# Performance work log

Hardware: AMD Instinct MI355X
Metric: run time of the kernel (lower is better)

Reference implementation:

```python
import jax, jax.numpy as jnp
import numpy as np

B, T, C, H = 2, 2048, 1024, 16
DK = DV = C // H  # 64
CONV_K = 4
EPS = 1e-5


def _causal_depthwise_conv(x, w):
    # x: [B, T, D], w: [D, K]; causal depthwise short convolution
    K = w.shape[1]
    xp = jnp.pad(x, ((0, 0), (K - 1, 0), (0, 0)))
    y = jax.lax.conv_general_dilated(
        xp.transpose(0, 2, 1), w[:, None, :], window_strides=(1,),
        padding='VALID', feature_group_count=w.shape[0])
    return y.transpose(0, 2, 1)


def _l2norm(x):
    return x * jax.lax.rsqrt(jnp.sum(x * x, axis=-1, keepdims=True) + 1e-6)


def _rope(x, rot_dim, base=10000.0):
    # x: [B, H, T, D]; rotate first rot_dim dims (partial_rotary_factor=0.5)
    t = x.shape[2]
    half = rot_dim // 2
    inv_freq = base ** (-jnp.arange(half, dtype=jnp.float32) / half)
    ang = jnp.arange(t, dtype=jnp.float32)[:, None] * inv_freq[None, :]
    cos, sin = jnp.cos(ang), jnp.sin(ang)
    x1 = x[..., :half]; x2 = x[..., half:rot_dim]; xpass = x[..., rot_dim:]
    return jnp.concatenate([x1 * cos - x2 * sin, x2 * cos + x1 * sin, xpass], axis=-1)


def setup_inputs() -> dict:
    key = jax.random.key(0)
    ks = jax.random.split(key, 16)
    s = 0.02
    inp = {
        'x': jax.random.normal(ks[0], (B, T, C), jnp.float32),
        'Wq': jax.random.normal(ks[1], (C, H * DK), jnp.float32) * s,
        'Wk': jax.random.normal(ks[2], (C, H * DK), jnp.float32) * s,
        'Wv': jax.random.normal(ks[3], (C, H * DV), jnp.float32) * s,
        'Wo': jax.random.normal(ks[4], (H * DV, C), jnp.float32) * s,
        'Wg': jax.random.normal(ks[5], (C, H * DV), jnp.float32) * s,
        'Wgk': jax.random.normal(ks[6], (C, H), jnp.float32) * s,
        'Wb': jax.random.normal(ks[7], (C, H), jnp.float32) * s,
        'bb': jnp.zeros((H,), jnp.float32),
        'A_log': jnp.log(jax.random.uniform(ks[8], (H,), jnp.float32, 0.5, 8.0)),
        'conv_q_w': jax.random.normal(ks[10], (H * DK, CONV_K), jnp.float32) * 0.2,
        'conv_k_w': jax.random.normal(ks[11], (H * DK, CONV_K), jnp.float32) * 0.2,
        'conv_v_w': jax.random.normal(ks[12], (H * DV, CONV_K), jnp.float32) * 0.2,
        'gnorm_w': jnp.ones((DV,), jnp.float32),
    }
    dt = jnp.exp(jax.random.uniform(ks[9], (H,), jnp.float32) * (np.log(0.1) - np.log(0.001)) + np.log(0.001))
    dt = jnp.clip(dt, 1e-4, None)
    inp['dt_bias'] = dt + jnp.log(-jnp.expm1(-dt))
    return inp


def reference(x, Wq, Wk, Wv, Wo, Wg, Wgk, Wb, bb, A_log, conv_q_w, conv_k_w, conv_v_w, gnorm_w, dt_bias):
    b, t, c = x.shape
    # projections + causal short conv + silu
    q = jax.nn.silu(_causal_depthwise_conv(x @ Wq, conv_q_w))
    k = jax.nn.silu(_causal_depthwise_conv(x @ Wk, conv_k_w))
    v = jax.nn.silu(_causal_depthwise_conv(x @ Wv, conv_v_w))
    # mamba-style per-head log forget gate and delta-rule learning rate beta
    gk = -jnp.exp(A_log) * jax.nn.softplus(x @ Wgk + dt_bias)   # [B, T, H]
    beta = jax.nn.sigmoid(x @ Wb + bb)                          # [B, T, H]
    q = q.reshape(b, t, H, DK).transpose(0, 2, 1, 3)
    k = k.reshape(b, t, H, DK).transpose(0, 2, 1, 3)
    v = v.reshape(b, t, H, DV).transpose(0, 2, 1, 3)
    q = _rope(_l2norm(q), DK // 2)
    k = _rope(_l2norm(k), DK // 2)
    # gated delta-rule recurrence: S_t = exp(g_t) S_{t-1} + k_t (beta_t (v_t - S^T k_t))^T
    def step(S, ins):
        q_t, k_t, v_t, g_t, b_t = ins
        S = S * jnp.exp(g_t)[..., None, None]
        pred = jnp.einsum('bhk,bhkv->bhv', k_t, S)
        delta = b_t[..., None] * (v_t - pred)
        S = S + k_t[..., None] * delta[..., None, :]
        o_t = jnp.einsum('bhk,bhkv->bhv', q_t, S)
        return S, o_t
    S0 = jnp.zeros((b, H, DK, DV), jnp.float32)
    ins = (q.transpose(2, 0, 1, 3), k.transpose(2, 0, 1, 3), v.transpose(2, 0, 1, 3),
           gk.transpose(1, 0, 2), beta.transpose(1, 0, 2))
    _, o = jax.lax.scan(step, S0, ins)          # o: [T, B, H, DV]
    o = o.transpose(1, 0, 2, 3)                 # [B, T, H, DV]
    # fused RMSNorm + swish gate, then output projection
    g = (x @ Wg).reshape(b, t, H, DV)
    o = o * jax.lax.rsqrt(jnp.mean(o * o, axis=-1, keepdims=True) + EPS)
    o = o * gnorm_w * jax.nn.silu(g)
    return o.reshape(b, t, H * DV) @ Wo
```

## Files before the change

kernel.cpp:

```cpp
#include <hip/hip_runtime.h>
#include <math.h>

typedef float f32x4 __attribute__((ext_vector_type(4)));
typedef __bf16 bf16x8 __attribute__((ext_vector_type(8)));
typedef __bf16 bf16x4 __attribute__((ext_vector_type(4)));

static constexpr int NB = 2, NT = 2048, NC = 1024, NH = 16, ND = 64;
static constexpr int NM = NB * NT;

__device__ inline float rdlane(float v, int l) {
  return __builtin_bit_cast(float, __builtin_amdgcn_readlane(__builtin_bit_cast(int, v), l));
}

__global__ __launch_bounds__(256) void k_convert(const float* __restrict__ src,
                                                 __bf16* __restrict__ dst, int n4) {
  int i = blockIdx.x * 256 + threadIdx.x;
  if (i >= n4) return;
  float4 v = ((const float4*)src)[i];
  bf16x4 o;
  o.x = (__bf16)v.x; o.y = (__bf16)v.y; o.z = (__bf16)v.z; o.w = (__bf16)v.w;
  ((bf16x4*)dst)[i] = o;
}

__global__ __launch_bounds__(256) void k_transpose(const float* __restrict__ src,
                                                   __bf16* __restrict__ dst) {
  __shared__ float t[64][65];
  int r0 = blockIdx.y * 64, c0 = blockIdx.x * 64;
  int lr = threadIdx.x >> 6;
  int lc = threadIdx.x & 63;
#pragma unroll
  for (int j = 0; j < 16; j++) {
    int r = j * 4 + lr;
    t[r][lc] = src[(size_t)(r0 + r) * 1024 + c0 + lc];
  }
  __syncthreads();
#pragma unroll
  for (int j = 0; j < 16; j++) {
    int r = j * 4 + lr;
    dst[(size_t)(c0 + r) * 1024 + r0 + lc] = (__bf16)t[lc][r];
  }
}

__global__ __launch_bounds__(256) void k_buildwgb(const float* __restrict__ Wgk,
    const float* __restrict__ Wb, __bf16* __restrict__ wgb_t) {
  int k0 = blockIdx.x * 64;
  int tid = threadIdx.x;
  int n = tid >> 3;
  int kk = (tid & 7) * 8;
  const float* src = n < 16 ? &Wgk[n] : &Wb[n - 16];
#pragma unroll
  for (int i = 0; i < 8; i++) {
    int k = k0 + kk + i;
    wgb_t[(size_t)n * 1024 + k] = (__bf16)src[(size_t)k * 16];
  }
  for (int i = tid; i < 6144; i += 256)
    wgb_t[32 * 1024 + (size_t)blockIdx.x * 6144 + i] = (__bf16)0.f;
}

__global__ __launch_bounds__(256) void k_gemm(const __bf16* __restrict__ A,
    const __bf16* B0, const __bf16* B1, const __bf16* B2, const __bf16* B3,
    const __bf16* B4, float* C0, float* C1, float* C2, float* C3, float* C4,
    int nblkPer) {
  constexpr int Kd = 1024;
  int mblk = blockIdx.x;
  int yb = blockIdx.y;
  int sel = yb / nblkPer;
  int nb = yb % nblkPer;
  const __bf16* Bt = sel == 0 ? B0 : sel == 1 ? B1 : sel == 2 ? B2 : sel == 3 ? B3 : B4;
  float* Cp = sel == 0 ? C0 : sel == 1 ? C1 : sel == 2 ? C2 : sel == 3 ? C3 : C4;
  int ldc = sel == 4 ? 128 : 1024;

  __shared__ __bf16 As[128 * 32];
  __shared__ __bf16 Bs[128 * 32];
  int tid = threadIdx.x;
  int lane = tid & 63;
  int w = tid >> 6;
  int wr = w >> 1, wc = w & 1;

  f32x4 acc[4][4];
#pragma unroll
  for (int r = 0; r < 4; r++)
#pragma unroll
    for (int c = 0; c < 4; c++) acc[r][c] = (f32x4){0.f, 0.f, 0.f, 0.f};

  int rowh = tid >> 2;
  int kcol = (tid & 3) * 8;
  const __bf16* aS = A + (size_t)(mblk * 128 + rowh) * Kd + kcol;
  const __bf16* bS = Bt + (size_t)(nb * 128 + rowh) * Kd + kcol;
  int rbase = (wr * 64 + (lane & 15)) * 32 + ((lane >> 4) * 8);
  int cbase = (wc * 64 + (lane & 15)) * 32 + ((lane >> 4) * 8);

  for (int kt = 0; kt < Kd; kt += 32) {
    uint4 a0 = *(const uint4*)(aS + kt);
    uint4 a1 = *(const uint4*)(aS + (size_t)64 * Kd + kt);
    uint4 b0 = *(const uint4*)(bS + kt);
    uint4 b1 = *(const uint4*)(bS + (size_t)64 * Kd + kt);
    __syncthreads();
    *(uint4*)&As[rowh * 32 + kcol] = a0;
    *(uint4*)&As[(rowh + 64) * 32 + kcol] = a1;
    *(uint4*)&Bs[rowh * 32 + kcol] = b0;
    *(uint4*)&Bs[(rowh + 64) * 32 + kcol] = b1;
    __syncthreads();
    bf16x8 af[4], bfr[4];
#pragma unroll
    for (int r = 0; r < 4; r++) af[r] = *(const bf16x8*)&As[rbase + r * 16 * 32];
#pragma unroll
    for (int c = 0; c < 4; c++) bfr[c] = *(const bf16x8*)&Bs[cbase + c * 16 * 32];
#pragma unroll
    for (int r = 0; r < 4; r++)
#pragma unroll
      for (int c = 0; c < 4; c++)
        acc[r][c] = __builtin_amdgcn_mfma_f32_16x16x32_bf16(af[r], bfr[c], acc[r][c], 0, 0, 0);
  }
  int orow = mblk * 128 + wr * 64 + ((lane >> 4) << 2);
  int ocol = nb * 128 + wc * 64 + (lane & 15);
#pragma unroll
  for (int r = 0; r < 4; r++)
#pragma unroll
    for (int c = 0; c < 4; c++)
#pragma unroll
      for (int j = 0; j < 4; j++)
        Cp[(size_t)(orow + r * 16 + j) * ldc + ocol + c * 16] = acc[r][c][j];
}

__global__ __launch_bounds__(256) void k_projpost(const float* __restrict__ pbuf,
    const float* __restrict__ bb, const float* __restrict__ A_log,
    const float* __restrict__ dtb, float* __restrict__ gk_arr,
    float* __restrict__ beta_arr) {
  int idx = blockIdx.x * 256 + threadIdx.x;
  int m = idx >> 5, j = idx & 31;
  int b = m >> 11, t = m & 2047;
  float v = pbuf[(size_t)m * 128 + j];
  if (j < 16) {
    float z = v + dtb[j];
    float sp = z > 20.f ? z : log1pf(__expf(z));
    gk_arr[((size_t)(b * 16 + j)) * 2048 + t] = -__expf(A_log[j]) * sp;
  } else {
    int jj = j - 16;
    float z = v + bb[jj];
    beta_arr[((size_t)(b * 16 + jj)) * 2048 + t] = 1.f / (1.f + __expf(-z));
  }
}

__global__ __launch_bounds__(256) void k_conv(
    const float* __restrict__ qpre, const float* __restrict__ kpre,
    const float* __restrict__ vpre, const float* __restrict__ cqw,
    const float* __restrict__ ckw, const float* __restrict__ cvw,
    float* __restrict__ qhat, float* __restrict__ khat, float* __restrict__ vhat) {
  int z = blockIdx.z;
  const float* src = z == 0 ? qpre : z == 1 ? kpre : vpre;
  const float* cw = z == 0 ? cqw : z == 1 ? ckw : cvw;
  float* dst = z == 0 ? qhat : z == 1 ? khat : vhat;
  int t0 = blockIdx.x * 64;
  int bh = blockIdx.y;
  int b = bh >> 4, h = bh & 15;
  int tid = threadIdx.x;
  __shared__ float tile[67 * 64];
  __shared__ float outb[64 * 64];
  for (int i = tid; i < 67 * 64; i += 256) {
    int r = i >> 6, c = i & 63;
    int t = t0 - 3 + r;
    tile[i] = (t >= 0) ? src[((size_t)(b * 2048 + t)) * 1024 + h * 64 + c] : 0.f;
  }
  __syncthreads();
  int c = tid & 63;
  int rb = (tid >> 6) * 16;
  float4 w4 = *(const float4*)&cw[(h * 64 + c) * 4];
  size_t obase = ((size_t)bh) * 2048 * 64;
#pragma unroll
  for (int rr = 0; rr < 16; rr++) {
    int r = rb + rr;
    float y = tile[r * 64 + c] * w4.x + tile[(r + 1) * 64 + c] * w4.y +
              tile[(r + 2) * 64 + c] * w4.z + tile[(r + 3) * 64 + c] * w4.w;
    float sv = y * (1.f / (1.f + __expf(-y)));
    if (z == 2) dst[obase + (size_t)(t0 + r) * 64 + c] = sv;
    else outb[r * 64 + c] = sv;
  }
  if (z == 2) return;
  __syncthreads();
  int r = tid >> 2;
  int p = tid & 3;
  float ss = 0.f;
#pragma unroll
  for (int i2 = 0; i2 < 16; i2++) { float vv = outb[r * 64 + p * 16 + i2]; ss += vv * vv; }
  ss += __shfl_xor(ss, 1);
  ss += __shfl_xor(ss, 2);
  float inv = rsqrtf(ss + 1e-6f);
  int tg = t0 + r;
#pragma unroll
  for (int i2 = 0; i2 < 16; i2++) {
    int cc = p * 16 + i2;
    float val = outb[r * 64 + cc] * inv;
    float res;
    if (cc < 16) {
      float x2 = outb[r * 64 + cc + 16] * inv;
      float ang = tg * __expf(-0.5756462732485114f * cc);
      float sn, cn; sincosf(ang, &sn, &cn);
      res = val * cn - x2 * sn;
    } else if (cc < 32) {
      float x1 = outb[r * 64 + cc - 16] * inv;
      float ang = tg * __expf(-0.5756462732485114f * (cc - 16));
      float sn, cn; sincosf(ang, &sn, &cn);
      res = val * cn + x1 * sn;
    } else res = val;
    dst[obase + (size_t)tg * 64 + cc] = res;
  }
}

__global__ __launch_bounds__(256) void k_chunkA(
    const float* __restrict__ khat, const float* __restrict__ vhat,
    const float* __restrict__ gk_arr, const float* __restrict__ beta_arr,
    float* __restrict__ cumbuf, float* __restrict__ Ubuf, float* __restrict__ Wbuf) {
  int bid = blockIdx.x;
  int bh = bid >> 5, ch = bid & 31;
  int tid = threadIdx.x;
  int lane = tid & 63, w = tid >> 6;
  __shared__ __bf16 Kbf[64 * 64];
  __shared__ __attribute__((aligned(16))) float Msh[64 * 68];
  __shared__ float cumsh[64], bsh[64];
  size_t kbase = (size_t)bh * (2048 * 64) + (size_t)ch * 4096;
  size_t gb = (size_t)bh * 2048 + ch * 64;
  size_t cb4096 = (size_t)(bh * 32 + ch) * 4096;

  {
    int row = tid >> 2, c16 = (tid & 3) * 16;
    const float* src = &khat[kbase + row * 64 + c16];
    float4 f0 = *(const float4*)(src + 0);
    float4 f1 = *(const float4*)(src + 4);
    float4 f2 = *(const float4*)(src + 8);
    float4 f3 = *(const float4*)(src + 12);
    bf16x8 h0, h1;
    h0[0] = (__bf16)f0.x; h0[1] = (__bf16)f0.y; h0[2] = (__bf16)f0.z; h0[3] = (__bf16)f0.w;
    h0[4] = (__bf16)f1.x; h0[5] = (__bf16)f1.y; h0[6] = (__bf16)f1.z; h0[7] = (__bf16)f1.w;
    h1[0] = (__bf16)f2.x; h1[1] = (__bf16)f2.y; h1[2] = (__bf16)f2.z; h1[3] = (__bf16)f2.w;
    h1[4] = (__bf16)f3.x; h1[5] = (__bf16)f3.y; h1[6] = (__bf16)f3.z; h1[7] = (__bf16)f3.w;
    int ch0 = ((c16 >> 3) + 0) ^ (row & 7);
    int ch1 = ((c16 >> 3) + 1) ^ (row & 7);
    *(bf16x8*)&Kbf[row * 64 + ch0 * 8] = h0;
    *(bf16x8*)&Kbf[row * 64 + ch1 * 8] = h1;
  }
  for (int i = tid; i < 64 * 68; i += 256) Msh[i] = 0.f;
  if (tid < 64) {
    float g = gk_arr[gb + tid];
    float bv = beta_arr[gb + tid];
#pragma unroll
    for (int d = 1; d < 64; d <<= 1) {
      float n = __shfl_up(g, d, 64);
      if (tid >= d) g += n;
    }
    cumsh[tid] = g;
    bsh[tid] = bv;
    cumbuf[(size_t)(bh * 32 + ch) * 64 + tid] = g;
  }
  __syncthreads();

  {
    f32x4 macc[4];
#pragma unroll
    for (int c = 0; c < 4; c++) macc[c] = (f32x4){0.f, 0.f, 0.f, 0.f};
    int arow = w * 16 + (lane & 15);
    int kb = lane >> 4;
    bf16x8 af0 = *(const bf16x8*)&Kbf[arow * 64 + ((0 + kb) ^ (arow & 7)) * 8];
    bf16x8 af1 = *(const bf16x8*)&Kbf[arow * 64 + ((4 + kb) ^ (arow & 7)) * 8];
#pragma unroll
    for (int c = 0; c < 4; c++) {
      if (c <= w) {
        int brow = c * 16 + (lane & 15);
        bf16x8 bf0 = *(const bf16x8*)&Kbf[brow * 64 + ((0 + kb) ^ (brow & 7)) * 8];
        bf16x8 bf1 = *(const bf16x8*)&Kbf[brow * 64 + ((4 + kb) ^ (brow & 7)) * 8];
        macc[c] = __builtin_amdgcn_mfma_f32_16x16x32_bf16(af0, bf0, macc[c], 0, 0, 0);
        macc[c] = __builtin_amdgcn_mfma_f32_16x16x32_bf16(af1, bf1, macc[c], 0, 0, 0);
      }
    }
    float bt[4], ct[4];
#pragma unroll
    for (int j = 0; j < 4; j++) {
      int trow = w * 16 + (lane >> 4) * 4 + j;
      bt[j] = bsh[trow];
      ct[j] = cumsh[trow];
    }
#pragma unroll
    for (int c = 0; c < 4; c++) {
      if (c <= w) {
        int scol = c * 16 + (lane & 15);
        float cums = cumsh[scol];
#pragma unroll
        for (int j = 0; j < 4; j++) {
          int trow = w * 16 + (lane >> 4) * 4 + j;
          float val = macc[c][j] * bt[j] * __expf(ct[j] - cums);
          Msh[trow * 68 + scol] = (scol < trow) ? val : 0.f;
        }
      }
    }
  }

  float uw[64];
  int c = tid;
  if (tid < 128) {
    bool isU = c < 64;
    int cc = c & 63;
    const float* src = isU ? &vhat[kbase + cc] : &khat[kbase + cc];
#pragma unroll
    for (int t = 0; t < 64; t++) {
      float r = src[t * 64] * bsh[t];
      if (!isU) r *= __expf(cumsh[t]);
      uw[t] = r;
    }
  }
  __syncthreads();

  if (tid < 128) {
#pragma unroll
    for (int t = 1; t < 64; t++) {
      float acc = 0.f;
#pragma unroll
      for (int q = 0; q <= (t - 1) >> 2; q++) {
        float4 m4 = *(const float4*)&Msh[t * 68 + q * 4];
        acc += m4.x * uw[q * 4 + 0] + m4.y * uw[q * 4 + 1] +
               m4.z * uw[q * 4 + 2] + m4.w * uw[q * 4 + 3];
      }
      uw[t] -= acc;
    }
    bool isU = c < 64;
    int cc = c & 63;
    float* dst = isU ? &Ubuf[cb4096 + cc] : &Wbuf[cb4096 + cc];
#pragma unroll
    for (int t = 0; t < 64; t++) dst[t * 64] = uw[t];
  }
}

__global__ __launch_bounds__(256) void k_chunkB(
    const float* __restrict__ khat, const float* __restrict__ cumbuf,
    const float* __restrict__ Ubuf, const float* __restrict__ Wbuf,
    float* __restrict__ Sch) {
  int bid = blockIdx.x;
  int bh = bid >> 3, vb = bid & 7;
  int tid = threadIdx.x;
  int lane = tid & 63, q_ = tid >> 6;
  int c0 = vb * 8 + q_ * 2;
  __shared__ float Ksh[64 * 68];
  float S0 = 0.f, S1 = 0.f;
  for (int ch = 0; ch < 32; ch++) {
    size_t cb = (size_t)(bh * 32 + ch);
    size_t kbase = (size_t)bh * (2048 * 64) + (size_t)ch * 4096;
    __syncthreads();
#pragma unroll
    for (int n4 = 0; n4 < 4; n4++) {
      int n = tid + n4 * 256;
      float4 kv = *(const float4*)&khat[kbase + (size_t)n * 4];
      int row = n >> 4, col = (n & 15) * 4;
      *(float4*)&Ksh[row * 68 + col] = kv;
    }
    float cumv = cumbuf[cb * 64 + lane];
    float cum63 = rdlane(cumv, 63);
    float sc = __expf(cum63 - cumv);
    float Gend = __expf(cum63);
    float2 uv = *(const float2*)&Ubuf[cb * 4096 + (size_t)lane * 64 + c0];
    float Wrow[64];
#pragma unroll
    for (int i4 = 0; i4 < 16; i4++) {
      float4 wv = *(const float4*)&Wbuf[cb * 4096 + (size_t)lane * 64 + i4 * 4];
      Wrow[i4 * 4 + 0] = wv.x; Wrow[i4 * 4 + 1] = wv.y;
      Wrow[i4 * 4 + 2] = wv.z; Wrow[i4 * 4 + 3] = wv.w;
    }
    Sch[cb * 4096 + (size_t)(c0 + 0) * 64 + lane] = S0;
    Sch[cb * 4096 + (size_t)(c0 + 1) * 64 + lane] = S1;
    float a0 = 0.f, a1 = 0.f;
#pragma unroll
    for (int i = 0; i < 64; i++) {
      float s0 = rdlane(S0, i), s1 = rdlane(S1, i);
      a0 += Wrow[i] * s0;
      a1 += Wrow[i] * s1;
    }
    float D0 = sc * (uv.x - a0);
    float D1 = sc * (uv.y - a1);
    __syncthreads();
    float n0 = 0.f, n1 = 0.f;
#pragma unroll
    for (int t = 0; t < 64; t++) {
      float d0 = rdlane(D0, t), d1 = rdlane(D1, t);
      float kk = Ksh[t * 68 + lane];
      n0 += kk * d0;
      n1 += kk * d1;
    }
    S0 = Gend * S0 + n0;
    S1 = Gend * S1 + n1;
  }
}

__global__ __launch_bounds__(256) void k_out(
    const float* __restrict__ qhat, const float* __restrict__ khat,
    const float* __restrict__ cumbuf, const float* __restrict__ Ubuf,
    const float* __restrict__ Wbuf, const float* __restrict__ Sch,
    float* __restrict__ o_pre) {
  int bid = blockIdx.x;
  int bh = bid >> 5, ch = bid & 31;
  int b = bh >> 4, h = bh & 15;
  int tid = threadIdx.x;
  __shared__ float B1[64][65];
  __shared__ float B2[64][65];
  __shared__ float B3[64][65];
  __shared__ float cumsh[64];
  size_t cb = (size_t)(bh * 32 + ch);
  size_t kbase = (size_t)bh * (2048 * 64) + (size_t)ch * 4096;
  if (tid < 64) cumsh[tid] = cumbuf[cb * 64 + tid];
  for (int idx = tid; idx < 4096; idx += 256) {
    B1[idx >> 6][idx & 63] = Wbuf[cb * 4096 + idx];
    B2[idx & 63][idx >> 6] = Sch[cb * 4096 + idx];
  }
  __syncthreads();
  int t_ = tid & 63, q_ = tid >> 6;
  int c0 = q_ * 16;
  float acc[16], o1[16], p[16];
#pragma unroll
  for (int j = 0; j < 16; j++) acc[j] = 0.f;
  for (int i = 0; i < 64; i++) {
    float w = B1[t_][i];
#pragma unroll
    for (int j = 0; j < 16; j++) acc[j] += w * B2[i][c0 + j];
  }
#pragma unroll
  for (int j = 0; j < 16; j += 4) {
    float4 u = *(const float4*)&Ubuf[cb * 4096 + (size_t)t_ * 64 + c0 + j];
    B3[t_][c0 + j + 0] = u.x - acc[j + 0];
    B3[t_][c0 + j + 1] = u.y - acc[j + 1];
    B3[t_][c0 + j + 2] = u.z - acc[j + 2];
    B3[t_][c0 + j + 3] = u.w - acc[j + 3];
  }
  __syncthreads();
  for (int idx = tid; idx < 4096; idx += 256)
    B1[idx >> 6][idx & 63] = qhat[kbase + idx];
  __syncthreads();
#pragma unroll
  for (int j = 0; j < 16; j++) o1[j] = 0.f;
  for (int i = 0; i < 64; i++) {
    float qv = B1[t_][i];
#pragma unroll
    for (int j = 0; j < 16; j++) o1[j] += qv * B2[i][c0 + j];
  }
  {
    float Gt = __expf(cumsh[t_]);
#pragma unroll
    for (int j = 0; j < 16; j++) o1[j] *= Gt;
  }
  __syncthreads();
  for (int idx = tid; idx < 4096; idx += 256)
    B2[idx >> 6][idx & 63] = khat[kbase + idx];
  __syncthreads();
#pragma unroll
  for (int m = 0; m < 16; m++) {
    int s = c0 + m;
    float d = 0.f;
    if (s <= t_) {
      for (int i = 0; i < 64; i++) d += B1[t_][i] * B2[s][i];
      d *= __expf(cumsh[t_] - cumsh[s]);
    }
    p[m] = d;
  }
  __syncthreads();
#pragma unroll
  for (int m = 0; m < 16; m++) B1[t_][c0 + m] = p[m];
  __syncthreads();
  for (int s = 0; s < 64; s++) {
    float pv = B1[t_][s];
#pragma unroll
    for (int j = 0; j < 16; j++) o1[j] += pv * B3[s][c0 + j];
  }
  size_t ob = ((size_t)(b * 2048 + ch * 64 + t_)) * 1024 + h * 64 + c0;
#pragma unroll
  for (int j = 0; j < 16; j += 4) {
    float4 o4 = {o1[j], o1[j + 1], o1[j + 2], o1[j + 3]};
    *(float4*)&o_pre[ob + j] = o4;
  }
}

__global__ __launch_bounds__(256) void k_gatenorm(const float* __restrict__ o_pre,
    const float* __restrict__ g, const float* __restrict__ gnw,
    __bf16* __restrict__ obf) {
  int m = blockIdx.x;
  int tid = threadIdx.x;
  size_t baseo = (size_t)m * 1024 + tid * 4;
  float4 ov = *(const float4*)&o_pre[baseo];
  float ss = ov.x * ov.x + ov.y * ov.y + ov.z * ov.z + ov.w * ov.w;
  ss += __shfl_xor(ss, 1);
  ss += __shfl_xor(ss, 2);
  ss += __shfl_xor(ss, 4);
  ss += __shfl_xor(ss, 8);
  float inv = rsqrtf(ss * (1.f / 64.f) + 1e-5f);
  float4 gv = *(const float4*)&g[baseo];
  int d0 = (tid & 15) * 4;
  float r0 = ov.x * inv * gnw[d0 + 0] * (gv.x * (1.f / (1.f + __expf(-gv.x))));
  float r1 = ov.y * inv * gnw[d0 + 1] * (gv.y * (1.f / (1.f + __expf(-gv.y))));
  float r2 = ov.z * inv * gnw[d0 + 2] * (gv.z * (1.f / (1.f + __expf(-gv.z))));
  float r3 = ov.w * inv * gnw[d0 + 3] * (gv.w * (1.f / (1.f + __expf(-gv.w))));
  bf16x4 o;
  o.x = (__bf16)r0; o.y = (__bf16)r1; o.z = (__bf16)r2; o.w = (__bf16)r3;
  *(bf16x4*)&obf[baseo] = o;
}

extern "C" void kernel_launch(void* const* d_in, const int* in_sizes, int n_in,
                              void* d_out, int out_size, void* d_ws, size_t ws_size,
                              hipStream_t stream) {
  const float* x = (const float*)d_in[0];
  const float* Wq = (const float*)d_in[1];
  const float* Wk = (const float*)d_in[2];
  const float* Wv = (const float*)d_in[3];
  const float* Wo = (const float*)d_in[4];
  const float* Wg = (const float*)d_in[5];
  const float* Wgk = (const float*)d_in[6];
  const float* Wb = (const float*)d_in[7];
  const float* bb = (const float*)d_in[8];
  const float* A_log = (const float*)d_in[9];
  const float* cqw = (const float*)d_in[10];
  const float* ckw = (const float*)d_in[11];
  const float* cvw = (const float*)d_in[12];
  const float* gnw = (const float*)d_in[13];
  const float* dtb = (const float*)d_in[14];
  float* out = (float*)d_out;

  char* ws = (char*)d_ws;
  __bf16* xbf   = (__bf16*)(ws + 0);
  __bf16* wq_t  = (__bf16*)(ws + 8388608);
  __bf16* wk_t  = (__bf16*)(ws + 10485760);
  __bf16* wv_t  = (__bf16*)(ws + 12582912);
  __bf16* wg_t  = (__bf16*)(ws + 14680064);
  __bf16* wo_t  = (__bf16*)(ws + 16777216);
  float* qpre   = (float*)(ws + 18874368);
  float* kpre   = (float*)(ws + 35651584);
  float* vpre   = (float*)(ws + 52428800);
  float* gbuf   = (float*)(ws + 69206016);
  float* qhat   = (float*)(ws + 85983232);
  float* khat   = (float*)(ws + 102760448);
  float* vhat   = (float*)(ws + 119537664);
  float* gk_arr = (float*)(ws + 136314880);
  float* beta_a = (float*)(ws + 136577024);
  float* o_pre  = qpre;
  __bf16* obf   = xbf;
  float* cumbuf = (float*)wq_t;
  float* Ubuf   = kpre;
  float* Wbuf   = vpre;
  float* Sch    = vhat;
  __bf16* wgb_t = (__bf16*)khat;
  float* pbuf   = qhat;

  k_convert<<<dim3((NM * NC / 4 + 255) / 256), 256, 0, stream>>>(x, xbf, NM * NC / 4);
  dim3 tg(16, 16);
  k_transpose<<<tg, 256, 0, stream>>>(Wq, wq_t);
  k_transpose<<<tg, 256, 0, stream>>>(Wk, wk_t);
  k_transpose<<<tg, 256, 0, stream>>>(Wv, wv_t);
  k_transpose<<<tg, 256, 0, stream>>>(Wg, wg_t);
  k_transpose<<<tg, 256, 0, stream>>>(Wo, wo_t);
  k_buildwgb<<<16, 256, 0, stream>>>(Wgk, Wb, wgb_t);
  k_gemm<<<dim3(NM / 128, 33), 256, 0, stream>>>(xbf, wq_t, wk_t, wv_t, wg_t, wgb_t,
                                                 qpre, kpre, vpre, gbuf, pbuf, 8);
  k_projpost<<<NM * 32 / 256, 256, 0, stream>>>(pbuf, bb, A_log, dtb, gk_arr, beta_a);
  k_conv<<<dim3(NT / 64, NB * NH, 3), 256, 0, stream>>>(qpre, kpre, vpre, cqw, ckw,
                                                        cvw, qhat, khat, vhat);
  k_chunkA<<<1024, 256, 0, stream>>>(khat, vhat, gk_arr, beta_a, cumbuf, Ubuf, Wbuf);
  k_chunkB<<<256, 256, 0, stream>>>(khat, cumbuf, Ubuf, Wbuf, Sch);
  k_out<<<1024, 256, 0, stream>>>(qhat, khat, cumbuf, Ubuf, Wbuf, Sch, o_pre);
  k_gatenorm<<<NM, 256, 0, stream>>>(o_pre, gbuf, gnw, obf);
  k_gemm<<<dim3(NM / 128, 8), 256, 0, stream>>>(obf, wo_t, nullptr, nullptr, nullptr,
                                                nullptr, out, nullptr, nullptr, nullptr,
                                                nullptr, 8);
}
```

Baseline: 499.0 us.

## Software-pipeline chunk state recurrence with double-buffered K tiles and prefetched W/U

```diff
diff --git a/kernel.cpp b/kernel.cpp
--- a/kernel.cpp
+++ b/kernel.cpp
@@ -329,6 +329,57 @@
   }
 }
 
+#define CHUNK_STEP(CH, WC, WN, UVC, UVN, CUMC, CUMN, CUR, NXT)                  \
+  {                                                                             \
+    size_t cb = cbb + (CH);                                                     \
+    int chn = (CH) < 31 ? (CH) + 1 : 31;                                        \
+    size_t cbn = cbb + chn;                                                     \
+                                 \
+    _Pragma("unroll")                                                           \
+    for (int i4 = 0; i4 < 16; i4++) {                                           \
+      float4 wv = *(const float4*)&Wbuf[cbn * 4096 + (size_t)lane * 64 + i4 * 4]; \
+      WN[i4 * 4 + 0] = wv.x; WN[i4 * 4 + 1] = wv.y;                             \
+      WN[i4 * 4 + 2] = wv.z; WN[i4 * 4 + 3] = wv.w;                             \
+    }                                                                           \
+    UVN = *(const float2*)&Ubuf[cbn * 4096 + (size_t)lane * 64 + c0];           \
+    CUMN = cumbuf[cbn * 64 + lane];                                             \
+    float4 knext[4];                                                            \
+    _Pragma("unroll")                                                           \
+    for (int n4 = 0; n4 < 4; n4++) {                                            \
+      int n = tid + n4 * 256;                                                   \
+      knext[n4] = *(const float4*)&khat[bhbase + (size_t)chn * 4096 + (size_t)n * 4]; \
+    }                                                                           \
+                                                     \
+    float cum63 = rdlane(CUMC, 63);                                             \
+    float sc = __expf(cum63 - CUMC);                                            \
+    float Gend = __expf(cum63);                                                 \
+    Sch[cb * 4096 + (size_t)(c0 + 0) * 64 + lane] = S0;                         \
+    Sch[cb * 4096 + (size_t)(c0 + 1) * 64 + lane] = S1;                         \
+    float a0 = 0.f, a1 = 0.f;                                                   \
+    _Pragma("unroll")                                                           \
+    for (int i = 0; i < 64; i++) {                                              \
+      float s0 = rdlane(S0, i), s1 = rdlane(S1, i);                             \
+      a0 += WC[i] * s0; a1 += WC[i] * s1;                                       \
+    }                                                                           \
+    float D0 = sc * (UVC.x - a0), D1 = sc * (UVC.y - a1);                       \
+    float n0 = 0.f, n1 = 0.f;                                                   \
+    _Pragma("unroll")                                                           \
+    for (int t = 0; t < 64; t++) {                                              \
+      float d0 = rdlane(D0, t), d1 = rdlane(D1, t);                             \
+      float kk = Ksh[CUR][t * 68 + lane];                                       \
+      n0 += kk * d0; n1 += kk * d1;                                             \
+    }                                                                           \
+    S0 = Gend * S0 + n0; S1 = Gend * S1 + n1;                                   \
+                                \
+    _Pragma("unroll")                                                           \
+    for (int n4 = 0; n4 < 4; n4++) {                                            \
+      int n = tid + n4 * 256;                                                   \
+      int row = n >> 4, col = (n & 15) * 4;                                     \
+      *(float4*)&Ksh[NXT][row * 68 + col] = knext[n4];                          \
+    }                                                                           \
+    __syncthreads();                                                            \
+  }
+
 __global__ __launch_bounds__(256) void k_chunkB(
     const float* __restrict__ khat, const float* __restrict__ cumbuf,
     const float* __restrict__ Ubuf, const float* __restrict__ Wbuf,
@@ -338,55 +389,43 @@
   int tid = threadIdx.x;
   int lane = tid & 63, q_ = tid >> 6;
   int c0 = vb * 8 + q_ * 2;
-  __shared__ float Ksh[64 * 68];
-  float S0 = 0.f, S1 = 0.f;
-  for (int ch = 0; ch < 32; ch++) {
-    size_t cb = (size_t)(bh * 32 + ch);
-    size_t kbase = (size_t)bh * (2048 * 64) + (size_t)ch * 4096;
-    __syncthreads();
+  __shared__ float Ksh[2][64 * 68];
+  size_t bhbase = (size_t)bh * (2048 * 64);
+  size_t cbb = (size_t)bh * 32;
+
+  float Wa[64], Wb[64];
+  float2 uva, uvb;
+  float cuma, cumb;
+#pragma unroll
+  for (int i4 = 0; i4 < 16; i4++) {
+    float4 wv = *(const float4*)&Wbuf[cbb * 4096 + (size_t)lane * 64 + i4 * 4];
+    Wa[i4 * 4 + 0] = wv.x; Wa[i4 * 4 + 1] = wv.y;
+    Wa[i4 * 4 + 2] = wv.z; Wa[i4 * 4 + 3] = wv.w;
+  }
+  uva = *(const float2*)&Ubuf[cbb * 4096 + (size_t)lane * 64 + c0];
+  cuma = cumbuf[cbb * 64 + lane];
+  {
+    float4 k0[4];
 #pragma unroll
     for (int n4 = 0; n4 < 4; n4++) {
       int n = tid + n4 * 256;
-      float4 kv = *(const float4*)&khat[kbase + (size_t)n * 4];
+      k0[n4] = *(const float4*)&khat[bhbase + (size_t)n * 4];
+    }
+#pragma unroll
+    for (int n4 = 0; n4 < 4; n4++) {
+      int n = tid + n4 * 256;
       int row = n >> 4, col = (n & 15) * 4;
-      *(float4*)&Ksh[row * 68 + col] = kv;
-    }
-    float cumv = cumbuf[cb * 64 + lane];
-    float cum63 = rdlane(cumv, 63);
-    float sc = __expf(cum63 - cumv);
-    float Gend = __expf(cum63);
-    float2 uv = *(const float2*)&Ubuf[cb * 4096 + (size_t)lane * 64 + c0];
-    float Wrow[64];
-#pragma unroll
-    for (int i4 = 0; i4 < 16; i4++) {
-      float4 wv = *(const float4*)&Wbuf[cb * 4096 + (size_t)lane * 64 + i4 * 4];
-      Wrow[i4 * 4 + 0] = wv.x; Wrow[i4 * 4 + 1] = wv.y;
-      Wrow[i4 * 4 + 2] = wv.z; Wrow[i4 * 4 + 3] = wv.w;
-    }
-    Sch[cb * 4096 + (size_t)(c0 + 0) * 64 + lane] = S0;
-    Sch[cb * 4096 + (size_t)(c0 + 1) * 64 + lane] = S1;
-    float a0 = 0.f, a1 = 0.f;
-#pragma unroll
-    for (int i = 0; i < 64; i++) {
-      float s0 = rdlane(S0, i), s1 = rdlane(S1, i);
-      a0 += Wrow[i] * s0;
-      a1 += Wrow[i] * s1;
-    }
-    float D0 = sc * (uv.x - a0);
-    float D1 = sc * (uv.y - a1);
-    __syncthreads();
-    float n0 = 0.f, n1 = 0.f;
-#pragma unroll
-    for (int t = 0; t < 64; t++) {
-      float d0 = rdlane(D0, t), d1 = rdlane(D1, t);
-      float kk = Ksh[t * 68 + lane];
-      n0 += kk * d0;
-      n1 += kk * d1;
-    }
-    S0 = Gend * S0 + n0;
-    S1 = Gend * S1 + n1;
-  }
-}
+      *(float4*)&Ksh[0][row * 68 + col] = k0[n4];
+    }
+  }
+  __syncthreads();
+  float S0 = 0.f, S1 = 0.f;
+  for (int ch = 0; ch < 32; ch += 2) {
+    CHUNK_STEP(ch, Wa, Wb, uva, uvb, cuma, cumb, 0, 1);
+    CHUNK_STEP(ch + 1, Wb, Wa, uvb, uva, cumb, cuma, 1, 0);
+  }
+}
+#undef CHUNK_STEP
 
 __global__ __launch_bounds__(256) void k_out(
     const float* __restrict__ qhat, const float* __restrict__ khat,
```

New measurement: 473.7 us. 1.05x faster.
